# Optimization experiments

Hardware: AMD Instinct MI355X
Metric: run time of the kernel (lower is better)

The kernel has to match this reference:

```python
import jax, jax.numpy as jnp
import numpy as np

IN_C, HID, LSTM_H, OUT_C = 128, 128, 128, 2
N_NODES, N_EDGES, N_GRAPHS = 100000, 1600000, 256


def gcn_conv(x, src, dst, W, b, n_nodes):
    # h = XW, then symmetric-normalized aggregation with self loops (PyG GCNConv defaults)
    h = x @ W  # [N, H]
    loop = jnp.arange(n_nodes)
    s = jnp.concatenate([src, loop])
    d = jnp.concatenate([dst, loop])
    deg = jax.ops.segment_sum(jnp.ones_like(d, dtype=h.dtype), d, num_segments=n_nodes)
    dinv = jnp.where(deg > 0, jax.lax.rsqrt(deg), 0.0)
    norm = dinv[s] * dinv[d]  # [E+N]
    out = jax.ops.segment_sum(norm[:, None] * h[s], d, num_segments=n_nodes)
    return out + b


def setup_inputs() -> dict:
    key = jax.random.key(0)
    ks = jax.random.split(key, 16)
    x = jax.random.normal(ks[0], (N_NODES, IN_C), dtype=jnp.float32)
    edge_index = jax.random.randint(ks[1], (2, N_EDGES), 0, N_NODES)
    batch = jnp.sort(jax.random.randint(ks[2], (N_NODES,), 0, N_GRAPHS))
    sc = lambda *shape: 1.0 / np.sqrt(shape[0])
    W0 = jax.random.normal(ks[3], (IN_C, HID), jnp.float32) * sc(IN_C)
    b0 = jnp.zeros((HID,), jnp.float32)
    W1 = jax.random.normal(ks[4], (HID, HID), jnp.float32) * sc(HID)
    b1 = jnp.zeros((HID,), jnp.float32)
    W2 = jax.random.normal(ks[5], (HID, HID), jnp.float32) * sc(HID)
    b2 = jnp.zeros((HID,), jnp.float32)
    W_ih = jax.random.normal(ks[6], (4 * LSTM_H, HID), jnp.float32) * sc(HID)
    W_hh = jax.random.normal(ks[7], (4 * LSTM_H, LSTM_H), jnp.float32) * sc(LSTM_H)
    b_ih = jnp.zeros((4 * LSTM_H,), jnp.float32)
    b_hh = jnp.zeros((4 * LSTM_H,), jnp.float32)
    W_fc = jax.random.normal(ks[8], (OUT_C, LSTM_H), jnp.float32) * sc(LSTM_H)
    b_fc = jnp.zeros((OUT_C,), jnp.float32)
    return dict(x=x, edge_index=edge_index, batch=batch, num_graphs=N_GRAPHS,
                W0=W0, b0=b0, W1=W1, b1=b1, W2=W2, b2=b2,
                W_ih=W_ih, W_hh=W_hh, b_ih=b_ih, b_hh=b_hh, W_fc=W_fc, b_fc=b_fc)


def reference(x, edge_index, batch, num_graphs, W0, b0, W1, b1, W2, b2,
              W_ih, W_hh, b_ih, b_hh, W_fc, b_fc):
    n_nodes = x.shape[0]
    src, dst = edge_index[0], edge_index[1]
    h = x
    for W, b in ((W0, b0), (W1, b1), (W2, b2)):
        h = jax.nn.relu(gcn_conv(h, src, dst, W, b, n_nodes))
    # dropout: identity in eval mode
    # global_mean_pool over batch ids
    sums = jax.ops.segment_sum(h, batch, num_segments=num_graphs)  # [G, HID]
    cnts = jax.ops.segment_sum(jnp.ones((n_nodes,), h.dtype), batch, num_segments=num_graphs)
    pooled = sums / jnp.maximum(cnts, 1.0)[:, None]
    # single-step LSTM from zero state: h0 = c0 = 0 => W_hh contributes 0
    g = pooled @ W_ih.T + b_ih + b_hh  # [G, 4H]
    i, f, gg, o = jnp.split(g, 4, axis=-1)  # PyTorch gate order i,f,g,o
    c = jax.nn.sigmoid(i) * jnp.tanh(gg)
    hn = jax.nn.sigmoid(o) * jnp.tanh(c)
    return hn @ W_fc.T + b_fc
```

## Files before the change

kernel.cpp:

```cpp
#include <hip/hip_runtime.h>
#include <math.h>
#include <stdint.h>

#define HID 128
#define SCAN_CHUNK 1024
#define NBUCK_MAX 512
#define EDGE_TILE 8192
#define GEMM_ROWS 128
#define XS_STRIDE 136

typedef short bf16x8 __attribute__((ext_vector_type(8)));
typedef float f32x4 __attribute__((ext_vector_type(4)));

__device__ __forceinline__ unsigned int f2bf(float f) {
    union { float f; uint32_t i; } u; u.f = f;
    uint32_t r = u.i + 0x7fffu + ((u.i >> 16) & 1u);
    return r >> 16;
}
__device__ __forceinline__ float bf2f_lo(uint32_t x) {
    union { uint32_t i; float f; } t; t.i = x << 16; return t.f;
}
__device__ __forceinline__ float bf2f_hi(uint32_t x) {
    union { uint32_t i; float f; } t; t.i = x & 0xffff0000u; return t.f;
}

__global__ __launch_bounds__(256) void scan_phase1(const int* __restrict__ cnt,
                                                   int* __restrict__ blockSums,
                                                   float* __restrict__ dinv, int nN) {
    __shared__ int sdata[256];
    const int t = threadIdx.x;
    const int idx = blockIdx.x * SCAN_CHUNK + t * 4;
    int v0 = 0, v1 = 0, v2 = 0, v3 = 0;
    if (idx + 3 < nN) {
        int4 v = *(const int4*)(cnt + idx);
        v0 = v.x; v1 = v.y; v2 = v.z; v3 = v.w;
        float4 dv;
        dv.x = rsqrtf((float)v0 + 1.0f);
        dv.y = rsqrtf((float)v1 + 1.0f);
        dv.z = rsqrtf((float)v2 + 1.0f);
        dv.w = rsqrtf((float)v3 + 1.0f);
        *(float4*)(dinv + idx) = dv;
    } else {
        if (idx     < nN) { v0 = cnt[idx];     dinv[idx]     = rsqrtf((float)v0 + 1.0f); }
        if (idx + 1 < nN) { v1 = cnt[idx + 1]; dinv[idx + 1] = rsqrtf((float)v1 + 1.0f); }
        if (idx + 2 < nN) { v2 = cnt[idx + 2]; dinv[idx + 2] = rsqrtf((float)v2 + 1.0f); }
        if (idx + 3 < nN) { v3 = cnt[idx + 3]; dinv[idx + 3] = rsqrtf((float)v3 + 1.0f); }
    }
    sdata[t] = v0 + v1 + v2 + v3;
    __syncthreads();
#pragma unroll
    for (int off = 128; off > 0; off >>= 1) {
        if (t < off) sdata[t] += sdata[t + off];
        __syncthreads();
    }
    if (t == 0) blockSums[blockIdx.x] = sdata[0];
}

__global__ __launch_bounds__(256) void scan_phase2(int* __restrict__ blockSums, int nB) {
    __shared__ int sd[256];
    const int t = threadIdx.x;
    sd[t] = (t < nB) ? blockSums[t] : 0;
    __syncthreads();
#pragma unroll
    for (int off = 1; off < 256; off <<= 1) {
        int v = sd[t];
        int add = (t >= off) ? sd[t - off] : 0;
        __syncthreads();
        sd[t] = v + add;
        __syncthreads();
    }
    if (t < nB) blockSums[t] = (t > 0) ? sd[t - 1] : 0;
}

__global__ __launch_bounds__(256) void scan_phase3(const int* __restrict__ cnt,
                                                   const int* __restrict__ blockOffsets,
                                                   int* __restrict__ rowptr, int nN, int nE) {
    __shared__ int sdata[256];
    const int t = threadIdx.x;
    const int idx = blockIdx.x * SCAN_CHUNK + t * 4;
    int v0 = 0, v1 = 0, v2 = 0, v3 = 0;
    if (idx + 3 < nN) {
        int4 v = *(const int4*)(cnt + idx);
        v0 = v.x; v1 = v.y; v2 = v.z; v3 = v.w;
    } else {
        if (idx     < nN) v0 = cnt[idx];
        if (idx + 1 < nN) v1 = cnt[idx + 1];
        if (idx + 2 < nN) v2 = cnt[idx + 2];
        if (idx + 3 < nN) v3 = cnt[idx + 3];
    }
    sdata[t] = v0 + v1 + v2 + v3;
    __syncthreads();
#pragma unroll
    for (int off = 1; off < 256; off <<= 1) {
        int v = sdata[t];
        int add = (t >= off) ? sdata[t - off] : 0;
        __syncthreads();
        sdata[t] = v + add;
        __syncthreads();
    }
    const int pre = blockOffsets[blockIdx.x] + ((t > 0) ? sdata[t - 1] : 0);
    if (idx + 3 < nN) {
        *(int4*)(rowptr + idx) = make_int4(pre, pre + v0, pre + v0 + v1, pre + v0 + v1 + v2);
    } else {
        if (idx     < nN) rowptr[idx]     = pre;
        if (idx + 1 < nN) rowptr[idx + 1] = pre + v0;
        if (idx + 2 < nN) rowptr[idx + 2] = pre + v0 + v1;
        if (idx + 3 < nN) rowptr[idx + 3] = pre + v0 + v1 + v2;
    }
    if (blockIdx.x == 0 && t == 0) rowptr[nN] = nE;
}

__global__ __launch_bounds__(256) void bucket_count(const int* __restrict__ dst,
                                                    int* __restrict__ bcnt, int nE, int nB) {
    __shared__ int h[NBUCK_MAX];
    for (int i = threadIdx.x; i < nB; i += 256) h[i] = 0;
    __syncthreads();
    const int base = blockIdx.x * EDGE_TILE;
    const int end = min(base + EDGE_TILE, nE);
    for (int e = base + threadIdx.x; e < end; e += 256)
        atomicAdd(&h[dst[e] >> 8], 1);
    __syncthreads();
    for (int i = threadIdx.x; i < nB; i += 256)
        if (h[i]) atomicAdd(&bcnt[i], h[i]);
}

__global__ __launch_bounds__(512) void bucket_scan(const int* __restrict__ bcnt,
                                                   int* __restrict__ boff,
                                                   int* __restrict__ bcur, int nB) {
    __shared__ int sd[512];
    const int t = threadIdx.x;
    sd[t] = (t < nB) ? bcnt[t] : 0;
    __syncthreads();
#pragma unroll
    for (int off = 1; off < 512; off <<= 1) {
        int v = sd[t];
        int add = (t >= off) ? sd[t - off] : 0;
        __syncthreads();
        sd[t] = v + add;
        __syncthreads();
    }
    if (t < nB) {
        int ex = (t > 0) ? sd[t - 1] : 0;
        boff[t] = ex;
        bcur[t] = ex;
    }
}

__global__ __launch_bounds__(256) void bucket_scatter(const int* __restrict__ src,
                                                      const int* __restrict__ dst,
                                                      int* __restrict__ bcur,
                                                      unsigned int* __restrict__ ebuf,
                                                      int nE, int nB) {
    __shared__ int h[NBUCK_MAX];
    __shared__ int basearr[NBUCK_MAX];
    const int base = blockIdx.x * EDGE_TILE;
    const int end = min(base + EDGE_TILE, nE);
    for (int i = threadIdx.x; i < nB; i += 256) h[i] = 0;
    __syncthreads();
    for (int e = base + threadIdx.x; e < end; e += 256)
        atomicAdd(&h[dst[e] >> 8], 1);
    __syncthreads();
    for (int i = threadIdx.x; i < nB; i += 256) {
        int c = h[i];
        basearr[i] = c ? atomicAdd(&bcur[i], c) : 0;
        h[i] = 0;
    }
    __syncthreads();
    for (int e = base + threadIdx.x; e < end; e += 256) {
        int d = dst[e];
        int b = d >> 8;
        int pos = basearr[b] + atomicAdd(&h[b], 1);
        ebuf[pos] = ((unsigned)src[e] << 8) | ((unsigned)d & 255u);
    }
}

__global__ __launch_bounds__(256) void node_count(const unsigned int* __restrict__ ebuf,
                                                  const int* __restrict__ boff,
                                                  int* __restrict__ cnt, int nE, int nB, int nN) {
    __shared__ int h[256];
    h[threadIdx.x] = 0;
    __syncthreads();
    const int b = blockIdx.x;
    const int e0 = boff[b];
    const int e1 = (b + 1 < nB) ? boff[b + 1] : nE;
    for (int e = e0 + threadIdx.x; e < e1; e += 256)
        atomicAdd(&h[ebuf[e] & 255u], 1);
    __syncthreads();
    const int v = b * 256 + threadIdx.x;
    if (v < nN) cnt[v] = h[threadIdx.x];
}

__global__ __launch_bounds__(256) void csr_from_buckets(const unsigned int* __restrict__ ebuf,
                                                        const int* __restrict__ boff,
                                                        const int* __restrict__ rowptr,
                                                        int* __restrict__ ssrc, int nE, int nB) {
    __shared__ int cur[256];
    const int b = blockIdx.x;
    const int e0 = boff[b];
    const int e1 = (b + 1 < nB) ? boff[b + 1] : nE;
    const int nodeBase = b * 256;
    cur[threadIdx.x] = 0;
    __syncthreads();
    for (int e = e0 + threadIdx.x; e < e1; e += 256) {
        unsigned int ed = ebuf[e];
        int li = (int)(ed & 255u);
        int pos = rowptr[nodeBase + li] + atomicAdd(&cur[li], 1);
        ssrc[pos] = (int)(ed >> 8);
    }
}

__global__ __launch_bounds__(256) void wt_kernel(const float* __restrict__ W0,
                                                 const float* __restrict__ W1,
                                                 const float* __restrict__ W2,
                                                 unsigned short* __restrict__ Wtb) {
    int i = blockIdx.x * 256 + threadIdx.x;
    if (i < 3 * HID * HID) {
        int w = i >> 14, r = i & 16383;
        int n = r >> 7, k = r & 127;
        const float* W = (w == 0) ? W0 : (w == 1) ? W1 : W2;
        Wtb[i] = (unsigned short)f2bf(W[k * HID + n]);
    }
}

__global__ __launch_bounds__(256) void gemm_mfma_f32in(const float* __restrict__ X,
                                                       const uint4* __restrict__ Wtb,
                                                       const float* __restrict__ dinv,
                                                       unsigned int* __restrict__ Pb32,
                                                       int nN) {
    __shared__ short Xs[GEMM_ROWS * XS_STRIDE];
    __shared__ short Ws[HID * XS_STRIDE];
    const int tid = threadIdx.x;
    const int rowBase = blockIdx.x * GEMM_ROWS;
#pragma unroll
    for (int it = 0; it < 16; ++it) {
        int f = it * 256 + tid;
        int row = f >> 5, c = f & 31;
        int grow = rowBase + row;
        float4 v = make_float4(0.f, 0.f, 0.f, 0.f);
        if (grow < nN) v = *(const float4*)(X + (size_t)grow * HID + c * 4);
        uint2 o;
        o.x = f2bf(v.x) | (f2bf(v.y) << 16);
        o.y = f2bf(v.z) | (f2bf(v.w) << 16);
        *(uint2*)(&Xs[row * XS_STRIDE + c * 4]) = o;
    }
#pragma unroll
    for (int it = 0; it < 8; ++it) {
        int f = it * 256 + tid;
        int n = f >> 4, c = f & 15;
        *(uint4*)(&Ws[n * XS_STRIDE + c * 8]) = Wtb[f];
    }
    __syncthreads();
    const int wave = tid >> 6, lane = tid & 63;
    const int quad = lane >> 4, l16 = lane & 15;
    f32x4 acc[2][8] = {};
    const int kq = quad * 8;
#pragma unroll
    for (int ks = 0; ks < 4; ++ks) {
        const int k0 = ks * 32 + kq;
        bf16x8 a0 = *(const bf16x8*)(&Xs[(wave * 32 + l16) * XS_STRIDE + k0]);
        bf16x8 a1 = *(const bf16x8*)(&Xs[(wave * 32 + 16 + l16) * XS_STRIDE + k0]);
#pragma unroll
        for (int nt = 0; nt < 8; ++nt) {
            bf16x8 b = *(const bf16x8*)(&Ws[(nt * 16 + l16) * XS_STRIDE + k0]);
            acc[0][nt] = __builtin_amdgcn_mfma_f32_16x16x32_bf16(a0, b, acc[0][nt], 0, 0, 0);
            acc[1][nt] = __builtin_amdgcn_mfma_f32_16x16x32_bf16(a1, b, acc[1][nt], 0, 0, 0);
        }
    }
#pragma unroll
    for (int mt = 0; mt < 2; ++mt) {
        const int gr0 = rowBase + wave * 32 + mt * 16 + quad * 4;
#pragma unroll
        for (int r = 0; r < 4; ++r) {
            const int gr = gr0 + r;
            const bool ok = gr < nN;
            const float d = ok ? dinv[gr] : 0.f;
#pragma unroll
            for (int nt = 0; nt < 8; ++nt) {
                float v = d * acc[mt][nt][r];
                float vo = __shfl_xor(v, 1, 64);
                if (ok && !(l16 & 1)) {
                    Pb32[(size_t)gr * 64 + nt * 8 + (l16 >> 1)] = f2bf(v) | (f2bf(vo) << 16);
                }
            }
        }
    }
}

__device__ __forceinline__ void acc_bf8(const uint4 q, float* a) {
    union { uint32_t i; float f; } t;
    t.i = q.x << 16;          a[0] += t.f;
    t.i = q.x & 0xffff0000u;  a[1] += t.f;
    t.i = q.y << 16;          a[2] += t.f;
    t.i = q.y & 0xffff0000u;  a[3] += t.f;
    t.i = q.z << 16;          a[4] += t.f;
    t.i = q.z & 0xffff0000u;  a[5] += t.f;
    t.i = q.w << 16;          a[6] += t.f;
    t.i = q.w & 0xffff0000u;  a[7] += t.f;
}

__global__ __launch_bounds__(256) void fused_agg_gemm(const uint4* __restrict__ Pb,
                                                      const int* __restrict__ rowptr,
                                                      const int* __restrict__ ssrc,
                                                      const float* __restrict__ dinv,
                                                      const float* __restrict__ bias,
                                                      const uint4* __restrict__ Wtb,
                                                      unsigned int* __restrict__ Pout32,
                                                      int nN) {
    __shared__ short Ws[HID * XS_STRIDE];
    __shared__ short Hs[16 * XS_STRIDE];
    const int tid = threadIdx.x;
#pragma unroll
    for (int it = 0; it < 8; ++it) {
        int f = it * 256 + tid;
        int n = f >> 4, c = f & 15;
        *(uint4*)(&Ws[n * XS_STRIDE + c * 8]) = Wtb[f];
    }
    const int lane16 = tid & 15;
    const int grp = tid >> 4;
    const int v = blockIdx.x * 16 + grp;
    const bool ok = v < nN;
    float a0[8], a1[8], a2[8], a3[8];
#pragma unroll
    for (int i = 0; i < 8; ++i) { a0[i] = 0.f; a1[i] = 0.f; a2[i] = 0.f; a3[i] = 0.f; }
    uint4 q = make_uint4(0u, 0u, 0u, 0u);
    if (ok) {
        acc_bf8(Pb[(size_t)v * 16 + lane16], a0);
        int e = rowptr[v];
        const int e1 = rowptr[v + 1];
        for (; e + 4 <= e1; e += 4) {
            const int u0 = ssrc[e + 0], u1 = ssrc[e + 1], u2 = ssrc[e + 2], u3 = ssrc[e + 3];
            uint4 q0 = Pb[(size_t)u0 * 16 + lane16];
            uint4 q1 = Pb[(size_t)u1 * 16 + lane16];
            uint4 q2 = Pb[(size_t)u2 * 16 + lane16];
            uint4 q3 = Pb[(size_t)u3 * 16 + lane16];
            acc_bf8(q0, a0); acc_bf8(q1, a1); acc_bf8(q2, a2); acc_bf8(q3, a3);
        }
        for (; e < e1; ++e) {
            uint4 qe = Pb[(size_t)ssrc[e] * 16 + lane16];
            acc_bf8(qe, a1);
        }
        const float dv = dinv[v];
        const float4 bb0 = ((const float4*)bias)[lane16 * 2];
        const float4 bb1 = ((const float4*)bias)[lane16 * 2 + 1];
        float4 o0, o1;
        o0.x = fmaxf(fmaf(dv, (a0[0] + a1[0]) + (a2[0] + a3[0]), bb0.x), 0.f);
        o0.y = fmaxf(fmaf(dv, (a0[1] + a1[1]) + (a2[1] + a3[1]), bb0.y), 0.f);
        o0.z = fmaxf(fmaf(dv, (a0[2] + a1[2]) + (a2[2] + a3[2]), bb0.z), 0.f);
        o0.w = fmaxf(fmaf(dv, (a0[3] + a1[3]) + (a2[3] + a3[3]), bb0.w), 0.f);
        o1.x = fmaxf(fmaf(dv, (a0[4] + a1[4]) + (a2[4] + a3[4]), bb1.x), 0.f);
        o1.y = fmaxf(fmaf(dv, (a0[5] + a1[5]) + (a2[5] + a3[5]), bb1.y), 0.f);
        o1.z = fmaxf(fmaf(dv, (a0[6] + a1[6]) + (a2[6] + a3[6]), bb1.z), 0.f);
        o1.w = fmaxf(fmaf(dv, (a0[7] + a1[7]) + (a2[7] + a3[7]), bb1.w), 0.f);
        q.x = f2bf(o0.x) | (f2bf(o0.y) << 16);
        q.y = f2bf(o0.z) | (f2bf(o0.w) << 16);
        q.z = f2bf(o1.x) | (f2bf(o1.y) << 16);
        q.w = f2bf(o1.z) | (f2bf(o1.w) << 16);
    }
    *(uint4*)(&Hs[grp * XS_STRIDE + lane16 * 8]) = q;
    __syncthreads();
    const int wave = tid >> 6, lane = tid & 63;
    const int quad = lane >> 4, l16 = lane & 15;
    f32x4 acc[2] = {};
#pragma unroll
    for (int ks = 0; ks < 4; ++ks) {
        const int k0 = ks * 32 + quad * 8;
        bf16x8 a = *(const bf16x8*)(&Hs[l16 * XS_STRIDE + k0]);
#pragma unroll
        for (int nt = 0; nt < 2; ++nt) {
            bf16x8 b = *(const bf16x8*)(&Ws[((wave * 2 + nt) * 16 + l16) * XS_STRIDE + k0]);
            acc[nt] = __builtin_amdgcn_mfma_f32_16x16x32_bf16(a, b, acc[nt], 0, 0, 0);
        }
    }
#pragma unroll
    for (int r = 0; r < 4; ++r) {
        const int gr = blockIdx.x * 16 + quad * 4 + r;
        const bool okr = gr < nN;
        const float d = okr ? dinv[gr] : 0.f;
#pragma unroll
        for (int nt = 0; nt < 2; ++nt) {
            float val = d * acc[nt][r];
            float vo = __shfl_xor(val, 1, 64);
            if (okr && !(l16 & 1)) {
                Pout32[(size_t)gr * 64 + (wave * 2 + nt) * 8 + (l16 >> 1)] =
                    f2bf(val) | (f2bf(vo) << 16);
            }
        }
    }
}

__global__ __launch_bounds__(256) void agg_pool(const uint4* __restrict__ Pb,
                                                const int* __restrict__ rowptr,
                                                const int* __restrict__ ssrc,
                                                const float* __restrict__ dinv,
                                                const float* __restrict__ bias,
                                                const int* __restrict__ batch,
                                                float* __restrict__ psum, int nN) {
    __shared__ float hsf[16][HID];
    __shared__ int sg[16];
    const int lane16 = threadIdx.x & 15;
    const int grp = threadIdx.x >> 4;
    const int v = blockIdx.x * 16 + grp;
    const bool ok = v < nN;
    float a0[8], a1[8], a2[8], a3[8];
#pragma unroll
    for (int i = 0; i < 8; ++i) { a0[i] = 0.f; a1[i] = 0.f; a2[i] = 0.f; a3[i] = 0.f; }
    float hv[8];
#pragma unroll
    for (int i = 0; i < 8; ++i) hv[i] = 0.f;
    if (ok) {
        acc_bf8(Pb[(size_t)v * 16 + lane16], a0);
        int e = rowptr[v];
        const int e1 = rowptr[v + 1];
        for (; e + 4 <= e1; e += 4) {
            const int u0 = ssrc[e + 0], u1 = ssrc[e + 1], u2 = ssrc[e + 2], u3 = ssrc[e + 3];
            uint4 q0 = Pb[(size_t)u0 * 16 + lane16];
            uint4 q1 = Pb[(size_t)u1 * 16 + lane16];
            uint4 q2 = Pb[(size_t)u2 * 16 + lane16];
            uint4 q3 = Pb[(size_t)u3 * 16 + lane16];
            acc_bf8(q0, a0); acc_bf8(q1, a1); acc_bf8(q2, a2); acc_bf8(q3, a3);
        }
        for (; e < e1; ++e) {
            uint4 q = Pb[(size_t)ssrc[e] * 16 + lane16];
            acc_bf8(q, a1);
        }
        const float dv = dinv[v];
        const float4 bb0 = ((const float4*)bias)[lane16 * 2];
        const float4 bb1 = ((const float4*)bias)[lane16 * 2 + 1];
        hv[0] = fmaxf(fmaf(dv, (a0[0] + a1[0]) + (a2[0] + a3[0]), bb0.x), 0.f);
        hv[1] = fmaxf(fmaf(dv, (a0[1] + a1[1]) + (a2[1] + a3[1]), bb0.y), 0.f);
        hv[2] = fmaxf(fmaf(dv, (a0[2] + a1[2]) + (a2[2] + a3[2]), bb0.z), 0.f);
        hv[3] = fmaxf(fmaf(dv, (a0[3] + a1[3]) + (a2[3] + a3[3]), bb0.w), 0.f);
        hv[4] = fmaxf(fmaf(dv, (a0[4] + a1[4]) + (a2[4] + a3[4]), bb1.x), 0.f);
        hv[5] = fmaxf(fmaf(dv, (a0[5] + a1[5]) + (a2[5] + a3[5]), bb1.y), 0.f);
        hv[6] = fmaxf(fmaf(dv, (a0[6] + a1[6]) + (a2[6] + a3[6]), bb1.z), 0.f);
        hv[7] = fmaxf(fmaf(dv, (a0[7] + a1[7]) + (a2[7] + a3[7]), bb1.w), 0.f);
    }
#pragma unroll
    for (int j = 0; j < 8; ++j) hsf[grp][lane16 * 8 + j] = hv[j];
    if (lane16 == 0) sg[grp] = ok ? batch[v] : -1;
    __syncthreads();
    if (threadIdx.x < HID) {
        const int c = threadIdx.x;
        float acc = 0.f;
        int g = sg[0];
#pragma unroll
        for (int i = 0; i < 16; ++i) {
            const int gi = sg[i];
            if (gi != g) {
                if (g >= 0) atomicAdd(&psum[(size_t)g * HID + c], acc);
                g = gi;
                acc = 0.f;
            }
            acc += hsf[i][c];
        }
        if (g >= 0) atomicAdd(&psum[(size_t)g * HID + c], acc);
    }
}

__global__ __launch_bounds__(128) void pool_lstm(const float* __restrict__ psum,
                                                 const int* __restrict__ batch,
                                                 const float* __restrict__ W_ih,
                                                 const float* __restrict__ b_ih,
                                                 const float* __restrict__ b_hh,
                                                 const float* __restrict__ W_fc,
                                                 const float* __restrict__ b_fc,
                                                 float* __restrict__ out, int nN) {
    __shared__ float pv[HID];
    __shared__ float r0[2], r1[2];
    __shared__ int scnt;
    const int g = blockIdx.x, j = threadIdx.x;
    if (j == 0) {
        int lo = 0, hi = nN;
        while (lo < hi) { int m = (lo + hi) >> 1; if (batch[m] < g) lo = m + 1; else hi = m; }
        const int start = lo;
        hi = nN;
        while (lo < hi) { int m = (lo + hi) >> 1; if (batch[m] < g + 1) lo = m + 1; else hi = m; }
        scnt = max(lo - start, 1);
    }
    __syncthreads();
    pv[j] = psum[(size_t)g * HID + j] / (float)scnt;
    __syncthreads();
    float di = b_ih[j] + b_hh[j];
    float dg = b_ih[256 + j] + b_hh[256 + j];
    float dO = b_ih[384 + j] + b_hh[384 + j];
    const float4* pv4 = (const float4*)pv;
#pragma unroll 4
    for (int k4 = 0; k4 < 32; ++k4) {
        float4 p = pv4[k4];
        float4 wi = *(const float4*)(W_ih + (size_t)j * HID + k4 * 4);
        float4 wg = *(const float4*)(W_ih + (size_t)(256 + j) * HID + k4 * 4);
        float4 wo = *(const float4*)(W_ih + (size_t)(384 + j) * HID + k4 * 4);
        di += p.x * wi.x + p.y * wi.y + p.z * wi.z + p.w * wi.w;
        dg += p.x * wg.x + p.y * wg.y + p.z * wg.z + p.w * wg.w;
        dO += p.x * wo.x + p.y * wo.y + p.z * wo.z + p.w * wo.w;
    }
    const float si = 1.0f / (1.0f + expf(-di));
    const float so = 1.0f / (1.0f + expf(-dO));
    const float c = si * tanhf(dg);
    const float hn = so * tanhf(c);
    float p0 = hn * W_fc[j];
    float p1 = hn * W_fc[HID + j];
#pragma unroll
    for (int off = 32; off > 0; off >>= 1) {
        p0 += __shfl_down(p0, off, 64);
        p1 += __shfl_down(p1, off, 64);
    }
    const int w = j >> 6, l = j & 63;
    if (l == 0) { r0[w] = p0; r1[w] = p1; }
    __syncthreads();
    if (j == 0) {
        out[g * 2 + 0] = r0[0] + r0[1] + b_fc[0];
        out[g * 2 + 1] = r1[0] + r1[1] + b_fc[1];
    }
}

extern "C" void kernel_launch(void* const* d_in, const int* in_sizes, int n_in,
                              void* d_out, int out_size, void* d_ws, size_t ws_size,
                              hipStream_t stream) {
    const float* x      = (const float*)d_in[0];
    const int*   eidx   = (const int*)d_in[1];
    const int*   batch  = (const int*)d_in[2];
    const float* W0     = (const float*)d_in[4];
    const float* b0     = (const float*)d_in[5];
    const float* W1     = (const float*)d_in[6];
    const float* b1     = (const float*)d_in[7];
    const float* W2     = (const float*)d_in[8];
    const float* b2     = (const float*)d_in[9];
    const float* W_ih   = (const float*)d_in[10];
    const float* b_ih   = (const float*)d_in[12];
    const float* b_hh   = (const float*)d_in[13];
    const float* W_fc   = (const float*)d_in[14];
    const float* b_fc   = (const float*)d_in[15];
    float* out = (float*)d_out;

    const int nN = in_sizes[0] / HID;
    const int nE = in_sizes[1] / 2;
    const int nG = out_size / 2;
    const int* src = eidx;
    const int* dst = eidx + nE;
    const int rowsPad = (nN + GEMM_ROWS - 1) & ~(GEMM_ROWS - 1);

    size_t off = 0;
    auto alloc = [&](size_t bytes) -> void* {
        void* p = (char*)d_ws + off;
        off += (bytes + 255) & ~(size_t)255;
        return p;
    };
    uint4* Pb     = (uint4*)alloc((size_t)nN * 16 * sizeof(uint4));
    uint4* Pb2    = (uint4*)alloc((size_t)nN * 16 * sizeof(uint4));
    float* dinv   = (float*)alloc((size_t)nN * sizeof(float));
    int*   cnt    = (int*)alloc((size_t)nN * sizeof(int));
    int*   rowptr = (int*)alloc((size_t)(nN + 1) * sizeof(int));
    int*   ssrc   = (int*)alloc((size_t)nE * sizeof(int));
    unsigned int* ebuf = (unsigned int*)alloc((size_t)nE * sizeof(unsigned int));
    float* psum   = (float*)alloc((size_t)nG * HID * sizeof(float));
    int*   blockSums = (int*)alloc(1024 * sizeof(int));
    int*   bcnt   = (int*)alloc(NBUCK_MAX * sizeof(int));
    int*   boff   = (int*)alloc(NBUCK_MAX * sizeof(int));
    int*   bcur   = (int*)alloc(NBUCK_MAX * sizeof(int));
    unsigned short* Wtb = (unsigned short*)alloc(3 * HID * HID * sizeof(unsigned short));
    (void)ws_size;

    const int scanBlocks = (nN + SCAN_CHUNK - 1) / SCAN_CHUNK;
    const int nB = (nN + 255) >> 8;
    const int tileBlocks = (nE + EDGE_TILE - 1) / EDGE_TILE;

    hipMemsetAsync(bcnt, 0, NBUCK_MAX * sizeof(int), stream);
    hipMemsetAsync(psum, 0, (size_t)nG * HID * sizeof(float), stream);
    bucket_count<<<tileBlocks, 256, 0, stream>>>(dst, bcnt, nE, nB);
    bucket_scan<<<1, 512, 0, stream>>>(bcnt, boff, bcur, nB);
    bucket_scatter<<<tileBlocks, 256, 0, stream>>>(src, dst, bcur, ebuf, nE, nB);

    node_count<<<nB, 256, 0, stream>>>(ebuf, boff, cnt, nE, nB, nN);
    scan_phase1<<<scanBlocks, 256, 0, stream>>>(cnt, blockSums, dinv, nN);
    scan_phase2<<<1, 256, 0, stream>>>(blockSums, scanBlocks);
    scan_phase3<<<scanBlocks, 256, 0, stream>>>(cnt, blockSums, rowptr, nN, nE);
    csr_from_buckets<<<nB, 256, 0, stream>>>(ebuf, boff, rowptr, ssrc, nE, nB);

    wt_kernel<<<(3 * HID * HID + 255) / 256, 256, 0, stream>>>(W0, W1, W2, Wtb);

    const int gemmBlocks = rowsPad / GEMM_ROWS;
    const int aggBlocks = (nN + 15) / 16;
    const uint4* Wt1 = (const uint4*)(Wtb + HID * HID);
    const uint4* Wt2 = (const uint4*)(Wtb + 2 * HID * HID);

    gemm_mfma_f32in<<<gemmBlocks, 256, 0, stream>>>(x, (const uint4*)Wtb, dinv,
                                                    (unsigned int*)Pb, nN);
    fused_agg_gemm<<<aggBlocks, 256, 0, stream>>>(Pb, rowptr, ssrc, dinv, b0, Wt1,
                                                  (unsigned int*)Pb2, nN);
    fused_agg_gemm<<<aggBlocks, 256, 0, stream>>>(Pb2, rowptr, ssrc, dinv, b1, Wt2,
                                                  (unsigned int*)Pb, nN);
    agg_pool<<<aggBlocks, 256, 0, stream>>>(Pb, rowptr, ssrc, dinv, b2, batch, psum, nN);

    pool_lstm<<<nG, 128, 0, stream>>>(psum, batch, W_ih, b_ih, b_hh, W_fc, b_fc,
                                      out, nN);
}
```

Before: 453.2 us.

## Fuse CSR build into one per-bucket kernel and fold weight transpose into bucket count

Node counting, the three-phase global scan, the dinv computation and the CSR scatter are merged into one per-bucket kernel. It uses the bucket offsets as each block's base and does a local 256-wide scan in shared memory. The bf16 weight transpose now runs inside the bucket count kernel, and the two memsets become one contiguous memset. Nontemporal loads and stores are added for edge indices, the X input and GEMM outputs. The aim is to cut several kernel launches and global round trips, at the risk of cache-hint side effects on the gather path.

Measured after the change: 467.3 us. +3.1%, slower.

```diff
diff --git a/kernel.cpp b/kernel.cpp
--- a/kernel.cpp
+++ b/kernel.cpp
@@ -3,7 +3,6 @@
 #include <stdint.h>
 
 #define HID 128
-#define SCAN_CHUNK 1024
 #define NBUCK_MAX 512
 #define EDGE_TILE 8192
 #define GEMM_ROWS 128
@@ -24,95 +23,21 @@
     union { uint32_t i; float f; } t; t.i = x & 0xffff0000u; return t.f;
 }
 
-__global__ __launch_bounds__(256) void scan_phase1(const int* __restrict__ cnt,
-                                                   int* __restrict__ blockSums,
-                                                   float* __restrict__ dinv, int nN) {
-    __shared__ int sdata[256];
-    const int t = threadIdx.x;
-    const int idx = blockIdx.x * SCAN_CHUNK + t * 4;
-    int v0 = 0, v1 = 0, v2 = 0, v3 = 0;
-    if (idx + 3 < nN) {
-        int4 v = *(const int4*)(cnt + idx);
-        v0 = v.x; v1 = v.y; v2 = v.z; v3 = v.w;
-        float4 dv;
-        dv.x = rsqrtf((float)v0 + 1.0f);
-        dv.y = rsqrtf((float)v1 + 1.0f);
-        dv.z = rsqrtf((float)v2 + 1.0f);
-        dv.w = rsqrtf((float)v3 + 1.0f);
-        *(float4*)(dinv + idx) = dv;
-    } else {
-        if (idx     < nN) { v0 = cnt[idx];     dinv[idx]     = rsqrtf((float)v0 + 1.0f); }
-        if (idx + 1 < nN) { v1 = cnt[idx + 1]; dinv[idx + 1] = rsqrtf((float)v1 + 1.0f); }
-        if (idx + 2 < nN) { v2 = cnt[idx + 2]; dinv[idx + 2] = rsqrtf((float)v2 + 1.0f); }
-        if (idx + 3 < nN) { v3 = cnt[idx + 3]; dinv[idx + 3] = rsqrtf((float)v3 + 1.0f); }
-    }
-    sdata[t] = v0 + v1 + v2 + v3;
-    __syncthreads();
-#pragma unroll
-    for (int off = 128; off > 0; off >>= 1) {
-        if (t < off) sdata[t] += sdata[t + off];
-        __syncthreads();
-    }
-    if (t == 0) blockSums[blockIdx.x] = sdata[0];
-}
-
-__global__ __launch_bounds__(256) void scan_phase2(int* __restrict__ blockSums, int nB) {
-    __shared__ int sd[256];
-    const int t = threadIdx.x;
-    sd[t] = (t < nB) ? blockSums[t] : 0;
-    __syncthreads();
-#pragma unroll
-    for (int off = 1; off < 256; off <<= 1) {
-        int v = sd[t];
-        int add = (t >= off) ? sd[t - off] : 0;
-        __syncthreads();
-        sd[t] = v + add;
-        __syncthreads();
-    }
-    if (t < nB) blockSums[t] = (t > 0) ? sd[t - 1] : 0;
-}
-
-__global__ __launch_bounds__(256) void scan_phase3(const int* __restrict__ cnt,
-                                                   const int* __restrict__ blockOffsets,
-                                                   int* __restrict__ rowptr, int nN, int nE) {
-    __shared__ int sdata[256];
-    const int t = threadIdx.x;
-    const int idx = blockIdx.x * SCAN_CHUNK + t * 4;
-    int v0 = 0, v1 = 0, v2 = 0, v3 = 0;
-    if (idx + 3 < nN) {
-        int4 v = *(const int4*)(cnt + idx);
-        v0 = v.x; v1 = v.y; v2 = v.z; v3 = v.w;
-    } else {
-        if (idx     < nN) v0 = cnt[idx];
-        if (idx + 1 < nN) v1 = cnt[idx + 1];
-        if (idx + 2 < nN) v2 = cnt[idx + 2];
-        if (idx + 3 < nN) v3 = cnt[idx + 3];
-    }
-    sdata[t] = v0 + v1 + v2 + v3;
-    __syncthreads();
-#pragma unroll
-    for (int off = 1; off < 256; off <<= 1) {
-        int v = sdata[t];
-        int add = (t >= off) ? sdata[t - off] : 0;
-        __syncthreads();
-        sdata[t] = v + add;
-        __syncthreads();
-    }
-    const int pre = blockOffsets[blockIdx.x] + ((t > 0) ? sdata[t - 1] : 0);
-    if (idx + 3 < nN) {
-        *(int4*)(rowptr + idx) = make_int4(pre, pre + v0, pre + v0 + v1, pre + v0 + v1 + v2);
-    } else {
-        if (idx     < nN) rowptr[idx]     = pre;
-        if (idx + 1 < nN) rowptr[idx + 1] = pre + v0;
-        if (idx + 2 < nN) rowptr[idx + 2] = pre + v0 + v1;
-        if (idx + 3 < nN) rowptr[idx + 3] = pre + v0 + v1 + v2;
-    }
-    if (blockIdx.x == 0 && t == 0) rowptr[nN] = nE;
-}
-
-__global__ __launch_bounds__(256) void bucket_count(const int* __restrict__ dst,
-                                                    int* __restrict__ bcnt, int nE, int nB) {
+__global__ __launch_bounds__(256) void bucket_count_wt(const int* __restrict__ dst,
+                                                       int* __restrict__ bcnt,
+                                                       const float* __restrict__ W0,
+                                                       const float* __restrict__ W1,
+                                                       const float* __restrict__ W2,
+                                                       unsigned short* __restrict__ Wtb,
+                                                       int nE, int nB) {
     __shared__ int h[NBUCK_MAX];
+    const int gid = blockIdx.x * 256 + threadIdx.x;
+    if (gid < 3 * HID * HID) {
+        int w = gid >> 14, r = gid & 16383;
+        int n = r >> 7, k = r & 127;
+        const float* W = (w == 0) ? W0 : (w == 1) ? W1 : W2;
+        Wtb[gid] = (unsigned short)f2bf(W[k * HID + n]);
+    }
     for (int i = threadIdx.x; i < nB; i += 256) h[i] = 0;
     __syncthreads();
     const int base = blockIdx.x * EDGE_TILE;
@@ -174,51 +99,49 @@
     }
 }
 
-__global__ __launch_bounds__(256) void node_count(const unsigned int* __restrict__ ebuf,
-                                                  const int* __restrict__ boff,
-                                                  int* __restrict__ cnt, int nE, int nB, int nN) {
+__global__ __launch_bounds__(256) void csr_build(const unsigned int* __restrict__ ebuf,
+                                                 const int* __restrict__ boff,
+                                                 float* __restrict__ dinv,
+                                                 int* __restrict__ rowptr,
+                                                 int* __restrict__ ssrc,
+                                                 int nE, int nB, int nN) {
     __shared__ int h[256];
-    h[threadIdx.x] = 0;
-    __syncthreads();
-    const int b = blockIdx.x;
+    __shared__ int rp[256];
+    const int b = blockIdx.x, t = threadIdx.x;
     const int e0 = boff[b];
     const int e1 = (b + 1 < nB) ? boff[b + 1] : nE;
-    for (int e = e0 + threadIdx.x; e < e1; e += 256)
+    h[t] = 0;
+    __syncthreads();
+    for (int e = e0 + t; e < e1; e += 256)
         atomicAdd(&h[ebuf[e] & 255u], 1);
     __syncthreads();
-    const int v = b * 256 + threadIdx.x;
-    if (v < nN) cnt[v] = h[threadIdx.x];
-}
-
-__global__ __launch_bounds__(256) void csr_from_buckets(const unsigned int* __restrict__ ebuf,
-                                                        const int* __restrict__ boff,
-                                                        const int* __restrict__ rowptr,
-                                                        int* __restrict__ ssrc, int nE, int nB) {
-    __shared__ int cur[256];
-    const int b = blockIdx.x;
-    const int e0 = boff[b];
-    const int e1 = (b + 1 < nB) ? boff[b + 1] : nE;
-    const int nodeBase = b * 256;
-    cur[threadIdx.x] = 0;
-    __syncthreads();
-    for (int e = e0 + threadIdx.x; e < e1; e += 256) {
+    const int c = h[t];
+    rp[t] = c;
+    __syncthreads();
+#pragma unroll
+    for (int off = 1; off < 256; off <<= 1) {
+        int v = rp[t];
+        int add = (t >= off) ? rp[t - off] : 0;
+        __syncthreads();
+        rp[t] = v + add;
+        __syncthreads();
+    }
+    const int pre = e0 + rp[t] - c;
+    const int v = b * 256 + t;
+    if (v < nN) {
+        rowptr[v] = pre;
+        dinv[v] = rsqrtf((float)c + 1.0f);
+    }
+    if (b == 0 && t == 0) rowptr[nN] = nE;
+    __syncthreads();
+    rp[t] = pre;
+    h[t] = 0;
+    __syncthreads();
+    for (int e = e0 + t; e < e1; e += 256) {
         unsigned int ed = ebuf[e];
         int li = (int)(ed & 255u);
-        int pos = rowptr[nodeBase + li] + atomicAdd(&cur[li], 1);
+        int pos = rp[li] + atomicAdd(&h[li], 1);
         ssrc[pos] = (int)(ed >> 8);
-    }
-}
-
-__global__ __launch_bounds__(256) void wt_kernel(const float* __restrict__ W0,
-                                                 const float* __restrict__ W1,
-                                                 const float* __restrict__ W2,
-                                                 unsigned short* __restrict__ Wtb) {
-    int i = blockIdx.x * 256 + threadIdx.x;
-    if (i < 3 * HID * HID) {
-        int w = i >> 14, r = i & 16383;
-        int n = r >> 7, k = r & 127;
-        const float* W = (w == 0) ? W0 : (w == 1) ? W1 : W2;
-        Wtb[i] = (unsigned short)f2bf(W[k * HID + n]);
     }
 }
 
@@ -236,11 +159,12 @@
         int f = it * 256 + tid;
         int row = f >> 5, c = f & 31;
         int grow = rowBase + row;
-        float4 v = make_float4(0.f, 0.f, 0.f, 0.f);
-        if (grow < nN) v = *(const float4*)(X + (size_t)grow * HID + c * 4);
+        f32x4 v = {0.f, 0.f, 0.f, 0.f};
+        if (grow < nN)
+            v = __builtin_nontemporal_load((const f32x4*)(X + (size_t)grow * HID + c * 4));
         uint2 o;
-        o.x = f2bf(v.x) | (f2bf(v.y) << 16);
-        o.y = f2bf(v.z) | (f2bf(v.w) << 16);
+        o.x = f2bf(v[0]) | (f2bf(v[1]) << 16);
+        o.y = f2bf(v[2]) | (f2bf(v[3]) << 16);
         *(uint2*)(&Xs[row * XS_STRIDE + c * 4]) = o;
     }
 #pragma unroll
@@ -328,7 +252,10 @@
         int e = rowptr[v];
         const int e1 = rowptr[v + 1];
         for (; e + 4 <= e1; e += 4) {
-            const int u0 = ssrc[e + 0], u1 = ssrc[e + 1], u2 = ssrc[e + 2], u3 = ssrc[e + 3];
+            const int u0 = __builtin_nontemporal_load(ssrc + e + 0);
+            const int u1 = __builtin_nontemporal_load(ssrc + e + 1);
+            const int u2 = __builtin_nontemporal_load(ssrc + e + 2);
+            const int u3 = __builtin_nontemporal_load(ssrc + e + 3);
             uint4 q0 = Pb[(size_t)u0 * 16 + lane16];
             uint4 q1 = Pb[(size_t)u1 * 16 + lane16];
             uint4 q2 = Pb[(size_t)u2 * 16 + lane16];
@@ -336,7 +263,8 @@
             acc_bf8(q0, a0); acc_bf8(q1, a1); acc_bf8(q2, a2); acc_bf8(q3, a3);
         }
         for (; e < e1; ++e) {
-            uint4 qe = Pb[(size_t)ssrc[e] * 16 + lane16];
+            const int u = __builtin_nontemporal_load(ssrc + e);
+            uint4 qe = Pb[(size_t)u * 16 + lane16];
             acc_bf8(qe, a1);
         }
         const float dv = dinv[v];
@@ -381,8 +309,9 @@
             float val = d * acc[nt][r];
             float vo = __shfl_xor(val, 1, 64);
             if (okr && !(l16 & 1)) {
-                Pout32[(size_t)gr * 64 + (wave * 2 + nt) * 8 + (l16 >> 1)] =
-                    f2bf(val) | (f2bf(vo) << 16);
+                __builtin_nontemporal_store(
+                    f2bf(val) | (f2bf(vo) << 16),
+                    Pout32 + (size_t)gr * 64 + (wave * 2 + nt) * 8 + (l16 >> 1));
             }
         }
     }
@@ -412,7 +341,10 @@
         int e = rowptr[v];
         const int e1 = rowptr[v + 1];
         for (; e + 4 <= e1; e += 4) {
-            const int u0 = ssrc[e + 0], u1 = ssrc[e + 1], u2 = ssrc[e + 2], u3 = ssrc[e + 3];
+            const int u0 = __builtin_nontemporal_load(ssrc + e + 0);
+            const int u1 = __builtin_nontemporal_load(ssrc + e + 1);
+            const int u2 = __builtin_nontemporal_load(ssrc + e + 2);
+            const int u3 = __builtin_nontemporal_load(ssrc + e + 3);
             uint4 q0 = Pb[(size_t)u0 * 16 + lane16];
             uint4 q1 = Pb[(size_t)u1 * 16 + lane16];
             uint4 q2 = Pb[(size_t)u2 * 16 + lane16];
@@ -420,7 +352,8 @@
             acc_bf8(q0, a0); acc_bf8(q1, a1); acc_bf8(q2, a2); acc_bf8(q3, a3);
         }
         for (; e < e1; ++e) {
-            uint4 q = Pb[(size_t)ssrc[e] * 16 + lane16];
+            const int u = __builtin_nontemporal_load(ssrc + e);
+            uint4 q = Pb[(size_t)u * 16 + lane16];
             acc_bf8(q, a1);
         }
         const float dv = dinv[v];
@@ -546,38 +479,30 @@
         off += (bytes + 255) & ~(size_t)255;
         return p;
     };
+    int*   bcnt   = (int*)alloc(NBUCK_MAX * sizeof(int));
+    float* psum   = (float*)alloc((size_t)nG * HID * sizeof(float));
     uint4* Pb     = (uint4*)alloc((size_t)nN * 16 * sizeof(uint4));
     uint4* Pb2    = (uint4*)alloc((size_t)nN * 16 * sizeof(uint4));
     float* dinv   = (float*)alloc((size_t)nN * sizeof(float));
-    int*   cnt    = (int*)alloc((size_t)nN * sizeof(int));
     int*   rowptr = (int*)alloc((size_t)(nN + 1) * sizeof(int));
     int*   ssrc   = (int*)alloc((size_t)nE * sizeof(int));
     unsigned int* ebuf = (unsigned int*)alloc((size_t)nE * sizeof(unsigned int));
-    float* psum   = (float*)alloc((size_t)nG * HID * sizeof(float));
-    int*   blockSums = (int*)alloc(1024 * sizeof(int));
-    int*   bcnt   = (int*)alloc(NBUCK_MAX * sizeof(int));
     int*   boff   = (int*)alloc(NBUCK_MAX * sizeof(int));
     int*   bcur   = (int*)alloc(NBUCK_MAX * sizeof(int));
     unsigned short* Wtb = (unsigned short*)alloc(3 * HID * HID * sizeof(unsigned short));
     (void)ws_size;
 
-    const int scanBlocks = (nN + SCAN_CHUNK - 1) / SCAN_CHUNK;
     const int nB = (nN + 255) >> 8;
     const int tileBlocks = (nE + EDGE_TILE - 1) / EDGE_TILE;
 
-    hipMemsetAsync(bcnt, 0, NBUCK_MAX * sizeof(int), stream);
-    hipMemsetAsync(psum, 0, (size_t)nG * HID * sizeof(float), stream);
-    bucket_count<<<tileBlocks, 256, 0, stream>>>(dst, bcnt, nE, nB);
+    hipMemsetAsync(bcnt, 0, NBUCK_MAX * sizeof(int) + (size_t)nG * HID * sizeof(float),
+                   stream);
+
+    bucket_count_wt<<<tileBlocks, 256, 0, stream>>>(dst, bcnt, W0, W1, W2, Wtb, nE, nB);
     bucket_scan<<<1, 512, 0, stream>>>(bcnt, boff, bcur, nB);
     bucket_scatter<<<tileBlocks, 256, 0, stream>>>(src, dst, bcur, ebuf, nE, nB);
 
-    node_count<<<nB, 256, 0, stream>>>(ebuf, boff, cnt, nE, nB, nN);
-    scan_phase1<<<scanBlocks, 256, 0, stream>>>(cnt, blockSums, dinv, nN);
-    scan_phase2<<<1, 256, 0, stream>>>(blockSums, scanBlocks);
-    scan_phase3<<<scanBlocks, 256, 0, stream>>>(cnt, blockSums, rowptr, nN, nE);
-    csr_from_buckets<<<nB, 256, 0, stream>>>(ebuf, boff, rowptr, ssrc, nE, nB);
-
-    wt_kernel<<<(3 * HID * HID + 255) / 256, 256, 0, stream>>>(W0, W1, W2, Wtb);
+    csr_build<<<nB, 256, 0, stream>>>(ebuf, boff, dinv, rowptr, ssrc, nE, nB, nN);
 
     const int gemmBlocks = rowsPad / GEMM_ROWS;
     const int aggBlocks = (nN + 15) / 16;
```
